# Performance work log

Hardware: AMD Instinct MI355X
Metric: run time of the kernel (lower is better)

The kernel has to match this reference:

```python
import jax, jax.numpy as jnp
import numpy as np

B, N, D, K, NUM_CLASSES = 8, 2048, 256, 8, 32
BN_EPS = 1e-5


def l2norm(x):
    return x / jnp.maximum(jnp.linalg.norm(x, axis=-1, keepdims=True), 1e-12)


def mlp2(x, W1, b1, W2, b2):
    # get_mlp([3, 32, D]): Linear -> ReLU -> Linear -> ReLU
    return jax.nn.relu(jax.nn.relu(x @ W1 + b1) @ W2 + b2)


def bn(x, g, b):
    # training-mode BatchNorm1d over all edges (flattened leading dims)
    ax = tuple(range(x.ndim - 1))
    m = jnp.mean(x, axis=ax, keepdims=True)
    v = jnp.var(x, axis=ax, keepdims=True)
    return (x - m) * jax.lax.rsqrt(v + BN_EPS) * g + b


def setup_inputs() -> dict:
    key = jax.random.key(0)
    ks = jax.random.split(key, 24)
    p = lambda i, shape: jax.random.normal(ks[i], shape, jnp.float32) * 0.05
    class_table = p(0, (NUM_CLASSES, D)).at[0].set(0.0)  # padding_idx=0
    return dict(
        class_idx=jax.random.randint(ks[1], (B, N), 0, NUM_CLASSES),
        colors=jax.random.uniform(ks[2], (B, N, 3), jnp.float32),
        positions=jax.random.normal(ks[3], (B, N, 3), jnp.float32),
        class_table=class_table,
        pos_W1=p(4, (3, 32)), pos_b1=p(5, (32,)),
        pos_W2=p(6, (32, D)), pos_b2=p(7, (D,)),
        col_W1=p(8, (3, 32)), col_b1=p(9, (32,)),
        col_W2=p(10, (32, D)), col_b2=p(11, (D,)),
        merge_W=p(12, (3 * D, D)), merge_b=p(13, (D,)),
        g_W1=p(14, (2 * D, D)), g_b1=p(15, (D,)),
        g_g1=jnp.ones((D,), jnp.float32), g_be1=jnp.zeros((D,), jnp.float32),
        g_W2=p(16, (D, D)), g_b2=p(17, (D,)),
        g_g2=jnp.ones((D,), jnp.float32), g_be2=jnp.zeros((D,), jnp.float32),
        lin_W1=p(18, (D, D)), lin_b1=p(19, (D,)),
        lin_W2=p(20, (D, D)), lin_b2=p(21, (D,)),
    )


def reference(class_idx, colors, positions, class_table,
              pos_W1, pos_b1, pos_W2, pos_b2,
              col_W1, col_b1, col_W2, col_b2,
              merge_W, merge_b,
              g_W1, g_b1, g_g1, g_be1, g_W2, g_b2, g_g2, g_be2,
              lin_W1, lin_b1, lin_W2, lin_b2):
    # --- per-object feature embeddings, each L2-normalized ---
    ce = l2norm(class_table[class_idx])                                   # [B,N,D]
    col = l2norm(mlp2(colors, col_W1, col_b1, col_W2, col_b2))            # [B,N,D]
    pos = l2norm(mlp2(positions, pos_W1, pos_b1, pos_W2, pos_b2))         # [B,N,D]
    x = jax.nn.relu(jnp.concatenate([ce, col, pos], -1) @ merge_W + merge_b)  # [B,N,D]
    # --- dynamic kNN in feature space, per sample (self edge included) ---
    sq = jnp.sum(x * x, -1)                                               # [B,N]
    d = sq[:, :, None] + sq[:, None, :] - 2.0 * jnp.einsum('bid,bjd->bij', x, x)
    _, idx = jax.lax.top_k(-jax.lax.stop_gradient(d), K)                  # [B,N,K]
    xj = jax.vmap(lambda e, i: e[i])(x, idx)                              # [B,N,K,D]
    xi = jnp.broadcast_to(x[:, :, None, :], xj.shape)
    e = jnp.concatenate([xi, xj - xi], -1)                                # [B,N,K,2D]
    # --- edge MLP [2D,D,D] with BN, max aggregation over neighbors ---
    h = bn(jax.nn.relu(e @ g_W1 + g_b1), g_g1, g_be1)
    h = bn(jax.nn.relu(h @ g_W2 + g_b2), g_g2, g_be2)
    node = jnp.max(h, axis=2)                                             # [B,N,D]
    pooled = jnp.max(node, axis=1)                                        # global_max_pool -> [B,D]
    out = jax.nn.relu(jax.nn.relu(pooled @ lin_W1 + lin_b1) @ lin_W2 + lin_b2)
    return l2norm(out)
```

## Files before the change

### kernel.cpp

```cpp
#include <hip/hip_runtime.h>
#include <math.h>

#define BB 8
#define NN 2048
#define DD 256
#define KNN 8
#define NPTS (BB*NN)
#define NEDGE (NPTS*KNN)
#define BN_EPS 1e-5f
#define NSH 64
#define PSH 32

#define OFF_X      0
#define OFF_FEAT   (OFF_X + NPTS*DD)
#define OFF_STATS  (OFF_FEAT + NPTS*3*DD)
#define OFF_PMAXS  (OFF_STATS + NSH*1024)
#define OFF_SQ     (OFF_PMAXS + PSH*BB*DD)
#define OFF_PMINS  (OFF_SQ + NPTS)
#define OFF_IDX    (OFF_PMINS + PSH*BB*DD)
#define OFF_U      (OFF_IDX + NEDGE)
#define OFF_V      (OFF_U + NPTS*DD)
#define OFF_W2BF   (OFF_V + NPTS*DD)
#define OFF_BIASP  (OFF_W2BF + 32768)
#define OFF_XHI    (OFF_BIASP + DD)
#define OFF_XLO    (OFF_XHI + NPTS*DD/2)

typedef __attribute__((ext_vector_type(8))) short bf16x8;
typedef __attribute__((ext_vector_type(4))) float f32x4;

__device__ __forceinline__ unsigned short f2bf(float f) {
  unsigned int u = __float_as_uint(f);
  u += 0x7FFF + ((u >> 16) & 1);
  return (unsigned short)(u >> 16);
}
__device__ __forceinline__ float bf2f(unsigned short h) {
  return __uint_as_float((unsigned int)h << 16);
}

__device__ __forceinline__ void gload_lds16(const float* g, float* lbase) {
#if defined(__has_builtin) && __has_builtin(__builtin_amdgcn_global_load_lds)
  __builtin_amdgcn_global_load_lds(
      (const __attribute__((address_space(1))) void*)(g),
      (__attribute__((address_space(3))) void*)(lbase),
      16, 0, 0);
#else
  int lane = threadIdx.x & 63;
  *(float4*)(lbase + lane*4) = *(const float4*)g;
#endif
}

__global__ __launch_bounds__(256) void featurize(
    const int* __restrict__ cls, const float* __restrict__ colors, const float* __restrict__ positions,
    const float* __restrict__ ctab,
    const float* __restrict__ pW1, const float* __restrict__ pb1, const float* __restrict__ pW2, const float* __restrict__ pb2,
    const float* __restrict__ cW1, const float* __restrict__ cb1, const float* __restrict__ cW2, const float* __restrict__ cb2,
    float* __restrict__ feat)
{
  __shared__ float wbuf[4][64];
  int tid = threadIdx.x;
  int wv = tid >> 6, lane = tid & 63;
  int p = blockIdx.x*4 + wv;
  if (lane < 32) {
    float c0 = colors[p*3+0], c1 = colors[p*3+1], c2 = colors[p*3+2];
    wbuf[wv][lane] = fmaxf(c0*cW1[lane] + c1*cW1[32+lane] + c2*cW1[64+lane] + cb1[lane], 0.f);
  } else {
    int l = lane - 32;
    float q0 = positions[p*3+0], q1 = positions[p*3+1], q2 = positions[p*3+2];
    wbuf[wv][32+l] = fmaxf(q0*pW1[l] + q1*pW1[32+l] + q2*pW1[64+l] + pb1[l], 0.f);
  }
  __syncthreads();
  int c = lane*4;
  float4 ce4 = *(const float4*)&ctab[(size_t)cls[p]*DD + c];
  float4 col4 = *(const float4*)&cb2[c];
  float4 pos4 = *(const float4*)&pb2[c];
  #pragma unroll
  for (int k = 0; k < 32; k++) {
    float ch = wbuf[wv][k], ph = wbuf[wv][32+k];
    float4 cw = *(const float4*)&cW2[k*DD + c];
    float4 pw = *(const float4*)&pW2[k*DD + c];
    col4.x += ch*cw.x; col4.y += ch*cw.y; col4.z += ch*cw.z; col4.w += ch*cw.w;
    pos4.x += ph*pw.x; pos4.y += ph*pw.y; pos4.z += ph*pw.z; pos4.w += ph*pw.w;
  }
  col4.x = fmaxf(col4.x, 0.f); col4.y = fmaxf(col4.y, 0.f);
  col4.z = fmaxf(col4.z, 0.f); col4.w = fmaxf(col4.w, 0.f);
  pos4.x = fmaxf(pos4.x, 0.f); pos4.y = fmaxf(pos4.y, 0.f);
  pos4.z = fmaxf(pos4.z, 0.f); pos4.w = fmaxf(pos4.w, 0.f);
  float sce  = ce4.x*ce4.x + ce4.y*ce4.y + ce4.z*ce4.z + ce4.w*ce4.w;
  float scol = col4.x*col4.x + col4.y*col4.y + col4.z*col4.z + col4.w*col4.w;
  float spos = pos4.x*pos4.x + pos4.y*pos4.y + pos4.z*pos4.z + pos4.w*pos4.w;
  #pragma unroll
  for (int m = 1; m <= 32; m <<= 1) {
    sce  += __shfl_xor(sce,  m, 64);
    scol += __shfl_xor(scol, m, 64);
    spos += __shfl_xor(spos, m, 64);
  }
  float ice = 1.f / fmaxf(sqrtf(sce),  1e-12f);
  float icl = 1.f / fmaxf(sqrtf(scol), 1e-12f);
  float ips = 1.f / fmaxf(sqrtf(spos), 1e-12f);
  float* fp = feat + (size_t)p*768;
  *(float4*)&fp[c]       = make_float4(ce4.x*ice,  ce4.y*ice,  ce4.z*ice,  ce4.w*ice);
  *(float4*)&fp[256 + c] = make_float4(col4.x*icl, col4.y*icl, col4.z*icl, col4.w*icl);
  *(float4*)&fp[512 + c] = make_float4(pos4.x*ips, pos4.y*ips, pos4.z*ips, pos4.w*ips);
}

__global__ __launch_bounds__(256) void gemm768(
    const float* __restrict__ A, const float* __restrict__ W, const float* __restrict__ bias,
    float* __restrict__ C, float* __restrict__ sqo,
    unsigned short* __restrict__ xhi, unsigned short* __restrict__ xlo)
{
  __shared__ float aT[32][68];
  __shared__ float bS[32*64];
  int tid = threadIdx.x;
  int tx = tid & 15, ty = tid >> 4;
  int rowbase = blockIdx.x * 64;
  int colbase = blockIdx.y * 64;
  int sr = tid >> 2, sk = (tid & 3) * 8;
  int lane = tid & 63, wv = tid >> 6;
  float acc[4][4] = {};
  for (int kc = 0; kc < 768; kc += 32) {
    const float* ap = A + (size_t)(rowbase + sr)*768 + kc + sk;
    float4 a0 = *(const float4*)ap;
    float4 a1 = *(const float4*)(ap + 4);
    __syncthreads();
    #pragma unroll
    for (int r = 0; r < 2; r++) {
      int R0 = r*16 + wv*4;
      gload_lds16(W + (size_t)(kc + R0 + (lane >> 4))*DD + colbase + (lane & 15)*4,
                  &bS[R0*64]);
    }
    aT[sk+0][sr]=a0.x; aT[sk+1][sr]=a0.y; aT[sk+2][sr]=a0.z; aT[sk+3][sr]=a0.w;
    aT[sk+4][sr]=a1.x; aT[sk+5][sr]=a1.y; aT[sk+6][sr]=a1.z; aT[sk+7][sr]=a1.w;
    __syncthreads();
    #pragma unroll
    for (int k = 0; k < 32; k++) {
      float4 av = *(const float4*)&aT[k][ty*4];
      float4 bv = *(const float4*)&bS[k*64 + tx*4];
      float a_[4] = {av.x, av.y, av.z, av.w};
      float b_[4] = {bv.x, bv.y, bv.z, bv.w};
      #pragma unroll
      for (int rr = 0; rr < 4; rr++)
        #pragma unroll
        for (int cc = 0; cc < 4; cc++)
          acc[rr][cc] += a_[rr]*b_[cc];
    }
  }
  float sqp[4];
  #pragma unroll
  for (int rr = 0; rr < 4; rr++) {
    int row = rowbase + ty*4 + rr;
    float o[4];
    unsigned short hi[4], lo[4];
    #pragma unroll
    for (int cc = 0; cc < 4; cc++) {
      float vv = acc[rr][cc] + bias[colbase + tx*4 + cc];
      o[cc] = fmaxf(vv, 0.f);
      hi[cc] = f2bf(o[cc]);
      lo[cc] = f2bf(o[cc] - bf2f(hi[cc]));
    }
    sqp[rr] = o[0]*o[0] + o[1]*o[1] + o[2]*o[2] + o[3]*o[3];
    *(float4*)&C[(size_t)row*DD + colbase + tx*4] = make_float4(o[0],o[1],o[2],o[3]);
    *(uint2*)&xhi[(size_t)row*DD + colbase + tx*4] =
        make_uint2((unsigned)hi[0] | ((unsigned)hi[1] << 16),
                   (unsigned)hi[2] | ((unsigned)hi[3] << 16));
    *(uint2*)&xlo[(size_t)row*DD + colbase + tx*4] =
        make_uint2((unsigned)lo[0] | ((unsigned)lo[1] << 16),
                   (unsigned)lo[2] | ((unsigned)lo[3] << 16));
  }
  #pragma unroll
  for (int rr = 0; rr < 4; rr++) {
    #pragma unroll
    for (int m = 1; m <= 8; m <<= 1) sqp[rr] += __shfl_xor(sqp[rr], m, 64);
  }
  if (tx == 0) {
    #pragma unroll
    for (int rr = 0; rr < 4; rr++)
      atomicAdd(&sqo[rowbase + ty*4 + rr], sqp[rr]);
  }
}

__global__ __launch_bounds__(256) void gemmuv(
    const float* __restrict__ A, const float* __restrict__ gW1,
    float* __restrict__ U, float* __restrict__ V)
{
  __shared__ float aT[32][68];
  __shared__ float bU[32][68];
  __shared__ float bV[32][68];
  int tid = threadIdx.x;
  int tx = tid & 15, ty = tid >> 4;
  int rowbase = blockIdx.x * 64;
  int colbase = blockIdx.y * 64;
  int sr = tid >> 2, sk = (tid & 3) * 8;
  float accU[4][4] = {}, accV[4][4] = {};
  for (int kc = 0; kc < DD; kc += 32) {
    const float* ap = A + (size_t)(rowbase + sr)*DD + kc + sk;
    float4 a0 = *(const float4*)ap;
    float4 a1 = *(const float4*)(ap + 4);
    const float* wt = gW1 + (size_t)(kc + ty)*DD + colbase + tx*4;
    const float* wb = wt + (size_t)DD*DD;
    float4 t0 = *(const float4*)wt;
    float4 t1 = *(const float4*)(wt + (size_t)16*DD);
    float4 o0 = *(const float4*)wb;
    float4 o1 = *(const float4*)(wb + (size_t)16*DD);
    __syncthreads();
    aT[sk+0][sr]=a0.x; aT[sk+1][sr]=a0.y; aT[sk+2][sr]=a0.z; aT[sk+3][sr]=a0.w;
    aT[sk+4][sr]=a1.x; aT[sk+5][sr]=a1.y; aT[sk+6][sr]=a1.z; aT[sk+7][sr]=a1.w;
    *(float4*)&bU[ty][tx*4]      = make_float4(t0.x-o0.x, t0.y-o0.y, t0.z-o0.z, t0.w-o0.w);
    *(float4*)&bU[ty + 16][tx*4] = make_float4(t1.x-o1.x, t1.y-o1.y, t1.z-o1.z, t1.w-o1.w);
    *(float4*)&bV[ty][tx*4]      = o0;
    *(float4*)&bV[ty + 16][tx*4] = o1;
    __syncthreads();
    #pragma unroll
    for (int k = 0; k < 32; k++) {
      float4 av = *(const float4*)&aT[k][ty*4];
      float4 bu = *(const float4*)&bU[k][tx*4];
      float4 bv = *(const float4*)&bV[k][tx*4];
      float a_[4] = {av.x, av.y, av.z, av.w};
      float u_[4] = {bu.x, bu.y, bu.z, bu.w};
      float v_[4] = {bv.x, bv.y, bv.z, bv.w};
      #pragma unroll
      for (int rr = 0; rr < 4; rr++)
        #pragma unroll
        for (int cc = 0; cc < 4; cc++) {
          accU[rr][cc] += a_[rr]*u_[cc];
          accV[rr][cc] += a_[rr]*v_[cc];
        }
    }
  }
  #pragma unroll
  for (int rr = 0; rr < 4; rr++) {
    int row = rowbase + ty*4 + rr;
    *(float4*)&U[(size_t)row*DD + colbase + tx*4] =
        make_float4(accU[rr][0], accU[rr][1], accU[rr][2], accU[rr][3]);
    *(float4*)&V[(size_t)row*DD + colbase + tx*4] =
        make_float4(accV[rr][0], accV[rr][1], accV[rr][2], accV[rr][3]);
  }
}

__global__ __launch_bounds__(256) void knnk(
    const unsigned short* __restrict__ xhi, const unsigned short* __restrict__ xlo,
    const float* __restrict__ sq,
    float* __restrict__ pdg, int* __restrict__ pjg)
{
  __shared__ float smem[4736];
  float* jh = smem;
  float* jl = smem + 2304;
  float (*dt)[65] = (float(*)[65])smem;
  float* sqI = smem + 4608;
  float* sqJ = smem + 4672;
  int tid = threadIdx.x;
  int q  = blockIdx.x & 3;
  int it = (blockIdx.x >> 2) & 31;
  int bb = blockIdx.x >> 7;
  int ibase = it * 64;
  const unsigned short* xhb = xhi + (size_t)bb*NN*DD;
  const unsigned short* xlb = xlo + (size_t)bb*NN*DD;
  const float* sqb = sq + (size_t)bb*NN;
  int w = tid >> 6, lane = tid & 63;
  int m = lane & 15, quad = lane >> 4;
  int selrow = tid & 63, selseg = tid >> 6;
  size_t aoff = (size_t)(ibase + w*16 + m)*DD;
  int srow = tid >> 2;
  int sseg = tid & 3;
  bf16x8 ahr[8], alr[8];
  #pragma unroll
  for (int c = 0; c < 8; c++) {
    int k0 = c*32 + quad*8;
    ahr[c] = *(const bf16x8*)(xhb + aoff + k0);
    alr[c] = *(const bf16x8*)(xlb + aoff + k0);
  }
  float bd[8]; int bj[8];
  #pragma unroll
  for (int s = 0; s < 8; s++) { bd[s] = 3.4e38f; bj[s] = 0; }
  if (tid < 64) sqI[tid] = sqb[ibase + tid];
  #pragma unroll 1
  for (int jt = 0; jt < 8; jt++) {
    int jbase = q*512 + jt*64;
    if (tid < 64) sqJ[tid] = sqb[jbase + tid];
    f32x4 acc[4];
    #pragma unroll
    for (int t = 0; t < 4; t++) acc[t] = (f32x4){0.f, 0.f, 0.f, 0.f};
    #pragma unroll
    for (int c2 = 0; c2 < 4; c2++) {
      size_t gb = (size_t)(jbase + srow)*DD + c2*64;
      float4 h0 = *(const float4*)((const float*)(xhb + gb) + sseg*4);
      float4 h1 = *(const float4*)((const float*)(xhb + gb) + (sseg+4)*4);
      float4 l0 = *(const float4*)((const float*)(xlb + gb) + sseg*4);
      float4 l1 = *(const float4*)((const float*)(xlb + gb) + (sseg+4)*4);
      __syncthreads();
      *(float4*)&jh[srow*36 + sseg*4]     = h0;
      *(float4*)&jh[srow*36 + (sseg+4)*4] = h1;
      *(float4*)&jl[srow*36 + sseg*4]     = l0;
      *(float4*)&jl[srow*36 + (sseg+4)*4] = l1;
      __syncthreads();
      #pragma unroll
      for (int kk = 0; kk < 2; kk++) {
        bf16x8 ah = ahr[c2*2 + kk];
        bf16x8 al = alr[c2*2 + kk];
        int lofs = kk*16 + quad*4;
        #pragma unroll
        for (int nt = 0; nt < 4; nt++) {
          int r = nt*16 + m;
          bf16x8 bh = *(const bf16x8*)&jh[r*36 + lofs];
          bf16x8 bl = *(const bf16x8*)&jl[r*36 + lofs];
          acc[nt] = __builtin_amdgcn_mfma_f32_16x16x32_bf16(ah, bh, acc[nt], 0, 0, 0);
          acc[nt] = __builtin_amdgcn_mfma_f32_16x16x32_bf16(ah, bl, acc[nt], 0, 0, 0);
          acc[nt] = __builtin_amdgcn_mfma_f32_16x16x32_bf16(al, bh, acc[nt], 0, 0, 0);
        }
      }
    }
    __syncthreads();
    #pragma unroll
    for (int nt = 0; nt < 4; nt++) {
      int col = nt*16 + m;
      float sj = sqJ[col];
      #pragma unroll
      for (int r = 0; r < 4; r++) {
        int rowl = w*16 + quad*4 + r;
        dt[rowl][col] = sqI[rowl] + sj - 2.f*acc[nt][r];
      }
    }
    __syncthreads();
    int cb = selseg*16;
    #pragma unroll
    for (int s = 0; s < 16; s++) {
      float dv = dt[selrow][cb + s];
      if (dv < bd[7]) {
        bd[7] = dv; bj[7] = jbase + cb + s;
        #pragma unroll
        for (int t = 7; t >= 1; t--) {
          if (bd[t] < bd[t-1]) {
            float td = bd[t]; bd[t] = bd[t-1]; bd[t-1] = td;
            int   tj = bj[t]; bj[t] = bj[t-1]; bj[t-1] = tj;
          }
        }
      }
    }
  }
  __syncthreads();
  float* pdl = &smem[0];
  int*   pjl = (int*)&smem[2048];
  #pragma unroll
  for (int s = 0; s < 8; s++) {
    pdl[tid*8 + s] = bd[s];
    pjl[tid*8 + s] = bj[s];
  }
  __syncthreads();
  if (tid < 64) {
    float md[8]; int mj[8];
    #pragma unroll
    for (int s = 0; s < 8; s++) { md[s] = 3.4e38f; mj[s] = 0; }
    #pragma unroll 1
    for (int g = 0; g < 4; g++) {
      int base = (g*64 + tid)*8;
      #pragma unroll
      for (int s = 0; s < 8; s++) {
        float dv = pdl[base + s];
        if (dv < md[7]) {
          md[7] = dv; mj[7] = pjl[base + s];
          #pragma unroll
          for (int t = 7; t >= 1; t--) {
            if (md[t] < md[t-1]) {
              float td = md[t]; md[t] = md[t-1]; md[t-1] = td;
              int   tj = mj[t]; mj[t] = mj[t-1]; mj[t-1] = tj;
            }
          }
        }
      }
    }
    size_t gbase = ((size_t)(bb*NN + ibase + tid))*32 + (size_t)q*8;
    #pragma unroll
    for (int s = 0; s < 8; s++) {
      pdg[gbase + s] = md[s];
      pjg[gbase + s] = bb*NN + mj[s];
    }
  }
}

__global__ __launch_bounds__(256) void knnmerge(const float* __restrict__ pdg, const int* __restrict__ pjg,
                                                int* __restrict__ idxg)
{
  int p = blockIdx.x*256 + threadIdx.x;
  float md[8]; int mj[8];
  #pragma unroll
  for (int s = 0; s < 8; s++) { md[s] = 3.4e38f; mj[s] = 0; }
  size_t base = (size_t)p*32;
  #pragma unroll 1
  for (int s = 0; s < 32; s++) {
    float dv = pdg[base + s];
    if (dv < md[7]) {
      md[7] = dv; mj[7] = pjg[base + s];
      #pragma unroll
      for (int t = 7; t >= 1; t--) {
        if (md[t] < md[t-1]) {
          float td = md[t]; md[t] = md[t-1]; md[t-1] = td;
          int   tj = mj[t]; mj[t] = mj[t-1]; mj[t-1] = tj;
        }
      }
    }
  }
  #pragma unroll
  for (int s = 0; s < 8; s++) idxg[(size_t)p*8 + s] = mj[s];
}

__global__ __launch_bounds__(256) void bn1stats(const float* __restrict__ u, const float* __restrict__ v,
    const int* __restrict__ idxg, const float* __restrict__ b1, float* __restrict__ stats)
{
  __shared__ int jL[128];
  int c = threadIdx.x;
  int n0 = blockIdx.x * 16;
  if (c < 128) jL[c] = idxg[(size_t)n0*8 + c];
  __syncthreads();
  float b1c = b1[c];
  float s = 0.f, s2 = 0.f;
  #pragma unroll 1
  for (int n = 0; n < 16; n++) {
    float uc = u[(size_t)(n0 + n)*DD + c];
    #pragma unroll
    for (int e = 0; e < 8; e++) {
      int j = jL[n*8 + e];
      float h = fmaxf(uc + v[(size_t)j*DD + c] + b1c, 0.f);
      s += h; s2 += h*h;
    }
  }
  int row = blockIdx.x & (NSH - 1);
  atomicAdd(&stats[row*1024 + c], s);
  atomicAdd(&stats[row*1024 + 256 + c], s2);
}

__global__ __launch_bounds__(256) void prep2(const float* __restrict__ stats, const float* __restrict__ g1,
    const float* __restrict__ be1, const float* __restrict__ gW2, const float* __restrict__ gb2,
    unsigned short* __restrict__ w2bf, float* __restrict__ biasp)
{
  __shared__ float s1L[256], t1L[256];
  int tid = threadIdx.x;
  const float inv = 1.f / (float)NEDGE;
  float sm = 0.f, sq2 = 0.f;
  #pragma unroll 1
  for (int r = 0; r < NSH; r++) {
    sm  += stats[r*1024 + tid];
    sq2 += stats[r*1024 + 256 + tid];
  }
  float m = sm * inv;
  float var = sq2*inv - m*m;
  float s1 = g1[tid] / sqrtf(var + BN_EPS);
  s1L[tid] = s1; t1L[tid] = be1[tid] - m*s1;
  __syncthreads();
  float bacc = gb2[tid];
  for (int k = 0; k < DD; k++) {
    float w = gW2[k*DD + tid];
    w2bf[(size_t)tid*DD + k] = f2bf(s1L[k]*w);
    bacc += t1L[k]*w;
  }
  biasp[tid] = bacc;
}

__global__ __launch_bounds__(256) void edgek(
    const float* __restrict__ u, const float* __restrict__ v, const int* __restrict__ idxg,
    const float* __restrict__ b1, const unsigned short* __restrict__ w2bf,
    const float* __restrict__ biasp,
    float* __restrict__ pmaxs, float* __restrict__ pmins, float* __restrict__ stats)
{
  __shared__ float wS[128*18];
  int tid = threadIdx.x;
  int w = tid >> 6, lane = tid & 63;
  int m = lane & 15, quad = lane >> 4;
  int rowbase = blockIdx.x * 64;
  int colbase = blockIdx.y * 128;
  int edge = rowbase + w*16 + m;
  int iu = edge >> 3;
  int jv = idxg[edge];
  const float* urow = u + (size_t)iu*DD;
  const float* vrow = v + (size_t)jv*DD;
  int srow = tid >> 1;
  int sseg = (tid & 1) * 2;
  f32x4 acc[8];
  #pragma unroll
  for (int t = 0; t < 8; t++) acc[t] = (f32x4){0.f, 0.f, 0.f, 0.f};
  #pragma unroll 1
  for (int c = 0; c < 8; c++) {
    int k0 = c*32 + quad*8;
    float4 ua = *(const float4*)(urow + k0);
    float4 ub = *(const float4*)(urow + k0 + 4);
    float4 va = *(const float4*)(vrow + k0);
    float4 vb = *(const float4*)(vrow + k0 + 4);
    float4 ba = *(const float4*)(b1 + k0);
    float4 bb = *(const float4*)(b1 + k0 + 4);
    const float* wrow = (const float*)(w2bf + (size_t)(colbase + srow)*DD + c*32);
    float4 wreg0 = *(const float4*)(wrow + sseg*4);
    float4 wreg1 = *(const float4*)(wrow + (sseg+1)*4);
    float h0 = fmaxf(ua.x+va.x+ba.x, 0.f);
    float h1 = fmaxf(ua.y+va.y+ba.y, 0.f);
    float h2 = fmaxf(ua.z+va.z+ba.z, 0.f);
    float h3 = fmaxf(ua.w+va.w+ba.w, 0.f);
    float h4 = fmaxf(ub.x+vb.x+bb.x, 0.f);
    float h5 = fmaxf(ub.y+vb.y+bb.y, 0.f);
    float h6 = fmaxf(ub.z+vb.z+bb.z, 0.f);
    float h7 = fmaxf(ub.w+vb.w+bb.w, 0.f);
    union { bf16x8 v8; unsigned short s[8]; } af;
    af.s[0] = f2bf(h0); af.s[1] = f2bf(h1); af.s[2] = f2bf(h2); af.s[3] = f2bf(h3);
    af.s[4] = f2bf(h4); af.s[5] = f2bf(h5); af.s[6] = f2bf(h6); af.s[7] = f2bf(h7);
    __syncthreads();
    *(float4*)&wS[srow*18 + sseg*4]     = wreg0;
    *(float4*)&wS[srow*18 + (sseg+1)*4] = wreg1;
    __syncthreads();
    #pragma unroll
    for (int nt = 0; nt < 8; nt++) {
      bf16x8 bf = *(const bf16x8*)&wS[(nt*16 + m)*18 + quad*4];
      acc[nt] = __builtin_amdgcn_mfma_f32_16x16x32_bf16(af.v8, bf, acc[nt], 0, 0, 0);
    }
  }
  float* redS = wS;
  float* redQ = wS + 512;
  float* redM = wS + 1024;
  float* redN = wS + 1536;
  float mxr[8], mnr[8], ssr[8], sqr[8];
  #pragma unroll
  for (int nt = 0; nt < 8; nt++) {
    int col = nt*16 + m;
    float bp = biasp[colbase + col];
    float r0 = fmaxf(acc[nt].x + bp, 0.f);
    float r1 = fmaxf(acc[nt].y + bp, 0.f);
    float r2 = fmaxf(acc[nt].z + bp, 0.f);
    float r3 = fmaxf(acc[nt].w + bp, 0.f);
    float mx = fmaxf(fmaxf(r0, r1), fmaxf(r2, r3));
    float mn = fminf(fminf(r0, r1), fminf(r2, r3));
    float ss = r0 + r1 + r2 + r3;
    float s2 = r0*r0 + r1*r1 + r2*r2 + r3*r3;
    mx = fmaxf(mx, __shfl_xor(mx, 16, 64));
    mx = fmaxf(mx, __shfl_xor(mx, 32, 64));
    mn = fminf(mn, __shfl_xor(mn, 16, 64));
    mn = fminf(mn, __shfl_xor(mn, 32, 64));
    ss += __shfl_xor(ss, 16, 64);
    ss += __shfl_xor(ss, 32, 64);
    s2 += __shfl_xor(s2, 16, 64);
    s2 += __shfl_xor(s2, 32, 64);
    mxr[nt] = mx; mnr[nt] = mn; ssr[nt] = ss; sqr[nt] = s2;
  }
  __syncthreads();
  if (quad == 0) {
    #pragma unroll
    for (int nt = 0; nt < 8; nt++) {
      int col = nt*16 + m;
      redS[w*128 + col] = ssr[nt];
      redQ[w*128 + col] = sqr[nt];
      redM[w*128 + col] = mxr[nt];
      redN[w*128 + col] = mnr[nt];
    }
  }
  __syncthreads();
  if (tid < 128) {
    float ts  = redS[tid] + redS[128+tid] + redS[256+tid] + redS[384+tid];
    float tq  = redQ[tid] + redQ[128+tid] + redQ[256+tid] + redQ[384+tid];
    float mxc = fmaxf(fmaxf(redM[tid], redM[128+tid]), fmaxf(redM[256+tid], redM[384+tid]));
    float mnc = fminf(fminf(redN[tid], redN[128+tid]), fminf(redN[256+tid], redN[384+tid]));
    int row = blockIdx.x & (NSH - 1);
    atomicAdd(&stats[row*1024 + 512 + colbase + tid], ts);
    atomicAdd(&stats[row*1024 + 768 + colbase + tid], tq);
    int b  = blockIdx.x >> 8;
    int sh = blockIdx.x & (PSH - 1);
    atomicMax((int*)&pmaxs[((size_t)sh*BB + b)*DD + colbase + tid], __float_as_int(mxc));
    atomicMin((int*)&pmins[((size_t)sh*BB + b)*DD + colbase + tid], __float_as_int(mnc));
  }
}

__global__ __launch_bounds__(256) void finalk(const float* __restrict__ pmaxs, const float* __restrict__ pmins,
    const float* __restrict__ stats, const float* __restrict__ g2, const float* __restrict__ be2,
    const float* __restrict__ W1, const float* __restrict__ b1,
    const float* __restrict__ W2, const float* __restrict__ b2,
    float* __restrict__ out)
{
  __shared__ float pl[256];
  __shared__ float hl[256];
  __shared__ float red[4];
  int c = threadIdx.x;
  int b = blockIdx.x;
  const float inv = 1.f / (float)NEDGE;
  float sm = 0.f, sq2 = 0.f;
  #pragma unroll 1
  for (int r = 0; r < NSH; r++) {
    sm  += stats[r*1024 + 512 + c];
    sq2 += stats[r*1024 + 768 + c];
  }
  float m = sm * inv;
  float var = sq2*inv - m*m;
  float s2 = g2[c] / sqrtf(var + BN_EPS);
  float t2 = be2[c] - m*s2;
  float mx = -3.4e38f, mn = 3.4e38f;
  #pragma unroll 1
  for (int s = 0; s < PSH; s++) {
    mx = fmaxf(mx, pmaxs[((size_t)s*BB + b)*DD + c]);
    mn = fminf(mn, pmins[((size_t)s*BB + b)*DD + c]);
  }
  pl[c] = (s2 >= 0.f) ? s2*mx + t2 : s2*mn + t2;
  __syncthreads();
  float h = b1[c];
  #pragma unroll 4
  for (int k = 0; k < 256; k++) h += pl[k]*W1[k*256 + c];
  hl[c] = fmaxf(h, 0.f);
  __syncthreads();
  float o = b2[c];
  #pragma unroll 4
  for (int k = 0; k < 256; k++) o += hl[k]*W2[k*256 + c];
  o = fmaxf(o, 0.f);
  float s = o*o;
  #pragma unroll
  for (int mm = 1; mm <= 32; mm <<= 1) s += __shfl_xor(s, mm, 64);
  if ((c & 63) == 0) red[c >> 6] = s;
  __syncthreads();
  float tot = red[0] + red[1] + red[2] + red[3];
  out[b*256 + c] = o / fmaxf(sqrtf(tot), 1e-12f);
}

extern "C" void kernel_launch(void* const* d_in, const int* in_sizes, int n_in,
                              void* d_out, int out_size, void* d_ws, size_t ws_size,
                              hipStream_t stream) {
  (void)in_sizes; (void)n_in; (void)out_size; (void)ws_size;
  const int*   cls       = (const int*)  d_in[0];
  const float* colors    = (const float*)d_in[1];
  const float* positions = (const float*)d_in[2];
  const float* ctab      = (const float*)d_in[3];
  const float* pW1 = (const float*)d_in[4];
  const float* pb1 = (const float*)d_in[5];
  const float* pW2 = (const float*)d_in[6];
  const float* pb2 = (const float*)d_in[7];
  const float* cW1 = (const float*)d_in[8];
  const float* cb1 = (const float*)d_in[9];
  const float* cW2 = (const float*)d_in[10];
  const float* cb2 = (const float*)d_in[11];
  const float* mW  = (const float*)d_in[12];
  const float* mb  = (const float*)d_in[13];
  const float* gW1 = (const float*)d_in[14];
  const float* gb1 = (const float*)d_in[15];
  const float* gg1 = (const float*)d_in[16];
  const float* gbe1= (const float*)d_in[17];
  const float* gW2 = (const float*)d_in[18];
  const float* gb2 = (const float*)d_in[19];
  const float* gg2 = (const float*)d_in[20];
  const float* gbe2= (const float*)d_in[21];
  const float* lW1 = (const float*)d_in[22];
  const float* lb1 = (const float*)d_in[23];
  const float* lW2 = (const float*)d_in[24];
  const float* lb2 = (const float*)d_in[25];
  float* out = (float*)d_out;

  float* wsf   = (float*)d_ws;
  float* x     = wsf + OFF_X;
  float* feat  = wsf + OFF_FEAT;
  float* sq    = wsf + OFF_SQ;
  int*   idxg  = (int*)(wsf + OFF_IDX);
  float* u     = wsf + OFF_U;
  float* v     = wsf + OFF_V;
  unsigned short* w2bf = (unsigned short*)(wsf + OFF_W2BF);
  float* biasp = wsf + OFF_BIASP;
  unsigned short* xhi = (unsigned short*)(wsf + OFF_XHI);
  unsigned short* xlo = (unsigned short*)(wsf + OFF_XLO);
  float* stats = wsf + OFF_STATS;
  float* pmaxs = wsf + OFF_PMAXS;
  float* pmins = wsf + OFF_PMINS;
  float* pdg   = feat;
  int*   pjg   = (int*)(feat + (size_t)NPTS*32);

  hipMemsetAsync(stats, 0, (NSH*1024 + PSH*BB*DD + NPTS)*sizeof(float), stream);
  hipMemsetAsync(pmins, 0x7f, PSH*BB*DD*sizeof(float), stream);

  featurize<<<NPTS/4, 256, 0, stream>>>(cls, colors, positions, ctab,
                                        pW1, pb1, pW2, pb2, cW1, cb1, cW2, cb2, feat);
  gemm768<<<dim3(NPTS/64, 4), 256, 0, stream>>>(feat, mW, mb, x, sq, xhi, xlo);
  knnk<<<BB*32*4, 256, 0, stream>>>(xhi, xlo, sq, pdg, pjg);
  knnmerge<<<NPTS/256, 256, 0, stream>>>(pdg, pjg, idxg);
  gemmuv<<<dim3(NPTS/64, 4), 256, 0, stream>>>(x, gW1, u, v);
  bn1stats<<<NPTS/16, 256, 0, stream>>>(u, v, idxg, gb1, stats);
  prep2<<<1, 256, 0, stream>>>(stats, gg1, gbe1, gW2, gb2, w2bf, biasp);
  edgek<<<dim3(NEDGE/64, 2), 256, 0, stream>>>(u, v, idxg, gb1, w2bf, biasp, pmaxs, pmins, stats);
  finalk<<<BB, 256, 0, stream>>>(pmaxs, pmins, stats, gg2, gbe2, lW1, lb1, lW2, lb2, out);
}
```

Before: 606.6 us.

## Run merge GEMM on bf16 MFMA with hi/lo split for fp32 accuracy

The 768-wide merge GEMM now runs on bf16 MFMA instructions instead of scalar fp32 FMAs. Features are written as bf16 hi/lo pairs, and the merge weights are split and transposed by a new prep kernel. Three MFMA products (hh, hl, lh) approximate fp32 precision. This adds a weight-prep launch and scattered scalar epilogue stores, in exchange for replacing the CUDA-core FMA work with matrix-core throughput.

```diff
diff --git a/kernel.cpp b/kernel.cpp
--- a/kernel.cpp
+++ b/kernel.cpp
@@ -24,6 +24,8 @@
 #define OFF_BIASP  (OFF_W2BF + 32768)
 #define OFF_XHI    (OFF_BIASP + DD)
 #define OFF_XLO    (OFF_XHI + NPTS*DD/2)
+#define OFF_MWH    (OFF_XLO + NPTS*DD/2)
+#define OFF_MWL    (OFF_MWH + 98304)
 
 typedef __attribute__((ext_vector_type(8))) short bf16x8;
 typedef __attribute__((ext_vector_type(4))) float f32x4;
@@ -35,18 +37,6 @@
 }
 __device__ __forceinline__ float bf2f(unsigned short h) {
   return __uint_as_float((unsigned int)h << 16);
-}
-
-__device__ __forceinline__ void gload_lds16(const float* g, float* lbase) {
-#if defined(__has_builtin) && __has_builtin(__builtin_amdgcn_global_load_lds)
-  __builtin_amdgcn_global_load_lds(
-      (const __attribute__((address_space(1))) void*)(g),
-      (__attribute__((address_space(3))) void*)(lbase),
-      16, 0, 0);
-#else
-  int lane = threadIdx.x & 63;
-  *(float4*)(lbase + lane*4) = *(const float4*)g;
-#endif
 }
 
 __global__ __launch_bounds__(256) void featurize(
@@ -54,7 +44,7 @@
     const float* __restrict__ ctab,
     const float* __restrict__ pW1, const float* __restrict__ pb1, const float* __restrict__ pW2, const float* __restrict__ pb2,
     const float* __restrict__ cW1, const float* __restrict__ cb1, const float* __restrict__ cW2, const float* __restrict__ cb2,
-    float* __restrict__ feat)
+    unsigned short* __restrict__ feathi, unsigned short* __restrict__ featlo)
 {
   __shared__ float wbuf[4][64];
   int tid = threadIdx.x;
@@ -97,84 +87,109 @@
   float ice = 1.f / fmaxf(sqrtf(sce),  1e-12f);
   float icl = 1.f / fmaxf(sqrtf(scol), 1e-12f);
   float ips = 1.f / fmaxf(sqrtf(spos), 1e-12f);
-  float* fp = feat + (size_t)p*768;
-  *(float4*)&fp[c]       = make_float4(ce4.x*ice,  ce4.y*ice,  ce4.z*ice,  ce4.w*ice);
-  *(float4*)&fp[256 + c] = make_float4(col4.x*icl, col4.y*icl, col4.z*icl, col4.w*icl);
-  *(float4*)&fp[512 + c] = make_float4(pos4.x*ips, pos4.y*ips, pos4.z*ips, pos4.w*ips);
+  float o[3][4] = {
+    {ce4.x*ice,  ce4.y*ice,  ce4.z*ice,  ce4.w*ice},
+    {col4.x*icl, col4.y*icl, col4.z*icl, col4.w*icl},
+    {pos4.x*ips, pos4.y*ips, pos4.z*ips, pos4.w*ips}
+  };
+  #pragma unroll
+  for (int sgm = 0; sgm < 3; sgm++) {
+    unsigned short h[4], l[4];
+    #pragma unroll
+    for (int cc = 0; cc < 4; cc++) {
+      h[cc] = f2bf(o[sgm][cc]);
+      l[cc] = f2bf(o[sgm][cc] - bf2f(h[cc]));
+    }
+    size_t off = (size_t)p*768 + sgm*256 + c;
+    *(uint2*)&feathi[off] = make_uint2((unsigned)h[0] | ((unsigned)h[1] << 16),
+                                       (unsigned)h[2] | ((unsigned)h[3] << 16));
+    *(uint2*)&featlo[off] = make_uint2((unsigned)l[0] | ((unsigned)l[1] << 16),
+                                       (unsigned)l[2] | ((unsigned)l[3] << 16));
+  }
+}
+
+__global__ __launch_bounds__(256) void prep_mw(const float* __restrict__ mW,
+    unsigned short* __restrict__ mwh, unsigned short* __restrict__ mwl)
+{
+  int k = blockIdx.x;
+  int n = threadIdx.x;
+  float wgt = mW[(size_t)k*DD + n];
+  unsigned short h = f2bf(wgt);
+  mwh[(size_t)n*768 + k] = h;
+  mwl[(size_t)n*768 + k] = f2bf(wgt - bf2f(h));
 }
 
 __global__ __launch_bounds__(256) void gemm768(
-    const float* __restrict__ A, const float* __restrict__ W, const float* __restrict__ bias,
-    float* __restrict__ C, float* __restrict__ sqo,
+    const unsigned short* __restrict__ feathi, const unsigned short* __restrict__ featlo,
+    const unsigned short* __restrict__ mwh, const unsigned short* __restrict__ mwl,
+    const float* __restrict__ mb,
+    float* __restrict__ x, float* __restrict__ sqo,
     unsigned short* __restrict__ xhi, unsigned short* __restrict__ xlo)
 {
-  __shared__ float aT[32][68];
-  __shared__ float bS[32*64];
+  __shared__ float wSh[128*18];
+  __shared__ float wSl[128*18];
   int tid = threadIdx.x;
-  int tx = tid & 15, ty = tid >> 4;
+  int w = tid >> 6, lane = tid & 63;
+  int m = lane & 15, quad = lane >> 4;
   int rowbase = blockIdx.x * 64;
-  int colbase = blockIdx.y * 64;
-  int sr = tid >> 2, sk = (tid & 3) * 8;
-  int lane = tid & 63, wv = tid >> 6;
-  float acc[4][4] = {};
-  for (int kc = 0; kc < 768; kc += 32) {
-    const float* ap = A + (size_t)(rowbase + sr)*768 + kc + sk;
-    float4 a0 = *(const float4*)ap;
-    float4 a1 = *(const float4*)(ap + 4);
-    __syncthreads();
-    #pragma unroll
-    for (int r = 0; r < 2; r++) {
-      int R0 = r*16 + wv*4;
-      gload_lds16(W + (size_t)(kc + R0 + (lane >> 4))*DD + colbase + (lane & 15)*4,
-                  &bS[R0*64]);
-    }
-    aT[sk+0][sr]=a0.x; aT[sk+1][sr]=a0.y; aT[sk+2][sr]=a0.z; aT[sk+3][sr]=a0.w;
-    aT[sk+4][sr]=a1.x; aT[sk+5][sr]=a1.y; aT[sk+6][sr]=a1.z; aT[sk+7][sr]=a1.w;
-    __syncthreads();
-    #pragma unroll
-    for (int k = 0; k < 32; k++) {
-      float4 av = *(const float4*)&aT[k][ty*4];
-      float4 bv = *(const float4*)&bS[k*64 + tx*4];
-      float a_[4] = {av.x, av.y, av.z, av.w};
-      float b_[4] = {bv.x, bv.y, bv.z, bv.w};
-      #pragma unroll
-      for (int rr = 0; rr < 4; rr++)
-        #pragma unroll
-        for (int cc = 0; cc < 4; cc++)
-          acc[rr][cc] += a_[rr]*b_[cc];
-    }
-  }
-  float sqp[4];
-  #pragma unroll
-  for (int rr = 0; rr < 4; rr++) {
-    int row = rowbase + ty*4 + rr;
-    float o[4];
-    unsigned short hi[4], lo[4];
-    #pragma unroll
-    for (int cc = 0; cc < 4; cc++) {
-      float vv = acc[rr][cc] + bias[colbase + tx*4 + cc];
-      o[cc] = fmaxf(vv, 0.f);
-      hi[cc] = f2bf(o[cc]);
-      lo[cc] = f2bf(o[cc] - bf2f(hi[cc]));
-    }
-    sqp[rr] = o[0]*o[0] + o[1]*o[1] + o[2]*o[2] + o[3]*o[3];
-    *(float4*)&C[(size_t)row*DD + colbase + tx*4] = make_float4(o[0],o[1],o[2],o[3]);
-    *(uint2*)&xhi[(size_t)row*DD + colbase + tx*4] =
-        make_uint2((unsigned)hi[0] | ((unsigned)hi[1] << 16),
-                   (unsigned)hi[2] | ((unsigned)hi[3] << 16));
-    *(uint2*)&xlo[(size_t)row*DD + colbase + tx*4] =
-        make_uint2((unsigned)lo[0] | ((unsigned)lo[1] << 16),
-                   (unsigned)lo[2] | ((unsigned)lo[3] << 16));
-  }
-  #pragma unroll
-  for (int rr = 0; rr < 4; rr++) {
-    #pragma unroll
-    for (int m = 1; m <= 8; m <<= 1) sqp[rr] += __shfl_xor(sqp[rr], m, 64);
-  }
-  if (tx == 0) {
-    #pragma unroll
-    for (int rr = 0; rr < 4; rr++)
-      atomicAdd(&sqo[rowbase + ty*4 + rr], sqp[rr]);
+  int colbase = blockIdx.y * 128;
+  size_t aoff = (size_t)(rowbase + w*16 + m)*768;
+  int srow = tid >> 1;
+  int sseg = (tid & 1) * 2;
+  f32x4 acc[8];
+  #pragma unroll
+  for (int t = 0; t < 8; t++) acc[t] = (f32x4){0.f, 0.f, 0.f, 0.f};
+  #pragma unroll 1
+  for (int c = 0; c < 24; c++) {
+    int k0 = c*32 + quad*8;
+    bf16x8 ah = *(const bf16x8*)(feathi + aoff + k0);
+    bf16x8 al = *(const bf16x8*)(featlo + aoff + k0);
+    const float* wrh = (const float*)(mwh + (size_t)(colbase + srow)*768 + c*32);
+    const float* wrl = (const float*)(mwl + (size_t)(colbase + srow)*768 + c*32);
+    float4 wh0 = *(const float4*)(wrh + sseg*4);
+    float4 wh1 = *(const float4*)(wrh + (sseg+1)*4);
+    float4 wl0 = *(const float4*)(wrl + sseg*4);
+    float4 wl1 = *(const float4*)(wrl + (sseg+1)*4);
+    __syncthreads();
+    *(float4*)&wSh[srow*18 + sseg*4]     = wh0;
+    *(float4*)&wSh[srow*18 + (sseg+1)*4] = wh1;
+    *(float4*)&wSl[srow*18 + sseg*4]     = wl0;
+    *(float4*)&wSl[srow*18 + (sseg+1)*4] = wl1;
+    __syncthreads();
+    #pragma unroll
+    for (int nt = 0; nt < 8; nt++) {
+      bf16x8 bh = *(const bf16x8*)&wSh[(nt*16 + m)*18 + quad*4];
+      bf16x8 bl = *(const bf16x8*)&wSl[(nt*16 + m)*18 + quad*4];
+      acc[nt] = __builtin_amdgcn_mfma_f32_16x16x32_bf16(ah, bh, acc[nt], 0, 0, 0);
+      acc[nt] = __builtin_amdgcn_mfma_f32_16x16x32_bf16(ah, bl, acc[nt], 0, 0, 0);
+      acc[nt] = __builtin_amdgcn_mfma_f32_16x16x32_bf16(al, bh, acc[nt], 0, 0, 0);
+    }
+  }
+  float sqp[4] = {0.f, 0.f, 0.f, 0.f};
+  #pragma unroll
+  for (int nt = 0; nt < 8; nt++) {
+    int col = colbase + nt*16 + m;
+    float bp = mb[col];
+    #pragma unroll
+    for (int r = 0; r < 4; r++) {
+      float o = fmaxf(acc[nt][r] + bp, 0.f);
+      int row = rowbase + w*16 + quad*4 + r;
+      x[(size_t)row*DD + col] = o;
+      unsigned short h = f2bf(o);
+      xhi[(size_t)row*DD + col] = h;
+      xlo[(size_t)row*DD + col] = f2bf(o - bf2f(h));
+      sqp[r] += o*o;
+    }
+  }
+  #pragma unroll
+  for (int r = 0; r < 4; r++) {
+    #pragma unroll
+    for (int mm = 1; mm <= 8; mm <<= 1) sqp[r] += __shfl_xor(sqp[r], mm, 64);
+  }
+  if (m == 0) {
+    #pragma unroll
+    for (int r = 0; r < 4; r++)
+      atomicAdd(&sqo[rowbase + w*16 + quad*4 + r], sqp[r]);
   }
 }
 
@@ -645,7 +660,8 @@
 
   float* wsf   = (float*)d_ws;
   float* x     = wsf + OFF_X;
-  float* feat  = wsf + OFF_FEAT;
+  unsigned short* feathi = (unsigned short*)(wsf + OFF_FEAT);
+  unsigned short* featlo = feathi + (size_t)NPTS*768;
   float* sq    = wsf + OFF_SQ;
   int*   idxg  = (int*)(wsf + OFF_IDX);
   float* u     = wsf + OFF_U;
@@ -654,18 +670,21 @@
   float* biasp = wsf + OFF_BIASP;
   unsigned short* xhi = (unsigned short*)(wsf + OFF_XHI);
   unsigned short* xlo = (unsigned short*)(wsf + OFF_XLO);
+  unsigned short* mwh = (unsigned short*)(wsf + OFF_MWH);
+  unsigned short* mwl = (unsigned short*)(wsf + OFF_MWL);
   float* stats = wsf + OFF_STATS;
   float* pmaxs = wsf + OFF_PMAXS;
   float* pmins = wsf + OFF_PMINS;
-  float* pdg   = feat;
-  int*   pjg   = (int*)(feat + (size_t)NPTS*32);
+  float* pdg   = wsf + OFF_FEAT;
+  int*   pjg   = (int*)(wsf + OFF_FEAT + (size_t)NPTS*32);
 
   hipMemsetAsync(stats, 0, (NSH*1024 + PSH*BB*DD + NPTS)*sizeof(float), stream);
   hipMemsetAsync(pmins, 0x7f, PSH*BB*DD*sizeof(float), stream);
 
   featurize<<<NPTS/4, 256, 0, stream>>>(cls, colors, positions, ctab,
-                                        pW1, pb1, pW2, pb2, cW1, cb1, cW2, cb2, feat);
-  gemm768<<<dim3(NPTS/64, 4), 256, 0, stream>>>(feat, mW, mb, x, sq, xhi, xlo);
+                                        pW1, pb1, pW2, pb2, cW1, cb1, cW2, cb2, feathi, featlo);
+  prep_mw<<<768, 256, 0, stream>>>(mW, mwh, mwl);
+  gemm768<<<dim3(NPTS/64, 2), 256, 0, stream>>>(feathi, featlo, mwh, mwl, mb, x, sq, xhi, xlo);
   knnk<<<BB*32*4, 256, 0, stream>>>(xhi, xlo, sq, pdg, pjg);
   knnmerge<<<NPTS/256, 256, 0, stream>>>(pdg, pjg, idxg);
   gemmuv<<<dim3(NPTS/64, 4), 256, 0, stream>>>(x, gW1, u, v);
```

Result: faster. 558.2 us (-8.0%).
